# Optimization experiments

Hardware: AMD Instinct MI355X
Metric: run time of the kernel (lower is better)

The kernel has to match this reference:

```python
import jax, jax.numpy as jnp
import numpy as np

DIM = 384
NUM_HEADS = 6
HEAD_DIM = DIM // NUM_HEADS
SCALE = HEAD_DIM ** -0.5


def setup_inputs() -> dict:
    key = jax.random.key(0)
    k_x, k_wqkv, k_bqkv, k_wp, k_bp = jax.random.split(key, 5)
    B, N, D = 16, 1024, DIM
    s = 0.02
    return {
        "x": jax.random.normal(k_x, (B, N, D), dtype=jnp.float32),
        "w_qkv": jax.random.normal(k_wqkv, (D, 3 * D), dtype=jnp.float32) * s,
        "b_qkv": jax.random.normal(k_bqkv, (3 * D,), dtype=jnp.float32) * s,
        "w_proj": jax.random.normal(k_wp, (D, D), dtype=jnp.float32) * s,
        "b_proj": jax.random.normal(k_bp, (D,), dtype=jnp.float32) * s,
    }


def reference(x, w_qkv, b_qkv, w_proj, b_proj):
    b, n, d = x.shape
    qkv = x @ w_qkv + b_qkv                               # (B, N, 3D)
    qkv = qkv.reshape(b, n, 3, NUM_HEADS, HEAD_DIM)
    qkv = jnp.transpose(qkv, (2, 0, 3, 1, 4))             # (3, B, H, N, hd)
    q, k, v = qkv[0], qkv[1], qkv[2]
    attn = jnp.einsum("bhqd,bhkd->bhqk", q, k) * SCALE    # (B, H, N, N)
    attn = jax.nn.softmax(attn, axis=-1)
    out = jnp.einsum("bhqk,bhkd->bhqd", attn, v)          # (B, H, N, hd)
    out = jnp.transpose(out, (0, 2, 1, 3)).reshape(b, n, d)
    return out @ w_proj + b_proj
```

## Files before the change

### kernel.cpp

```cpp
#include <hip/hip_runtime.h>

typedef __attribute__((ext_vector_type(8))) short short8;
typedef __attribute__((ext_vector_type(4))) float float4_t;
typedef __attribute__((ext_vector_type(4))) unsigned int uint4_t;

#define MFMA16(A, B, C) __builtin_amdgcn_mfma_f32_16x16x32_bf16(A, B, C, 0, 0, 0)

#define QSCALE 0.1803368801111168f

__device__ __forceinline__ unsigned short f2bf(float f) {
  unsigned int u = __builtin_bit_cast(unsigned int, f);
  u += 0x7FFFu + ((u >> 16) & 1u);
  return (unsigned short)(u >> 16);
}

__device__ __forceinline__ void gload16(const unsigned short* g, unsigned short* l) {
  __builtin_amdgcn_global_load_lds(
      (const __attribute__((address_space(1))) unsigned int*)(g),
      (__attribute__((address_space(3))) unsigned int*)(l), 16, 0, 0);
}

__global__ __launch_bounds__(256) void prep(
    const float* __restrict__ w_qkv, const float* __restrict__ w_proj,
    unsigned short* __restrict__ wqkvT, unsigned short* __restrict__ wprojT) {
  __shared__ unsigned short tile[32][33];
  const int bid = blockIdx.x, tid = threadIdx.x;
  const float* w; unsigned short* wT; int E, t;
  if (bid < 432) { t = bid; w = w_qkv; wT = wqkvT; E = 1152; }
  else           { t = bid - 432; w = w_proj; wT = wprojT; E = 384; }
  const int tiles_e = E >> 5;
  const int td = t / tiles_e, te = t - td * tiles_e;
  const int r = tid >> 3, c4 = (tid & 7) * 4;
  float4 v = *reinterpret_cast<const float4*>(&w[(size_t)(td * 32 + r) * E + te * 32 + c4]);
  tile[r][c4 + 0] = f2bf(v.x);
  tile[r][c4 + 1] = f2bf(v.y);
  tile[r][c4 + 2] = f2bf(v.z);
  tile[r][c4 + 3] = f2bf(v.w);
  __syncthreads();
  ushort4 o;
  o.x = tile[c4 + 0][r]; o.y = tile[c4 + 1][r];
  o.z = tile[c4 + 2][r]; o.w = tile[c4 + 3][r];
  *reinterpret_cast<ushort4*>(&wT[(size_t)(te * 32 + r) * 384 + td * 32 + c4]) = o;
}

__global__ __launch_bounds__(256, 3) void gemm_qkv(
    const float* __restrict__ x,
    const unsigned short* __restrict__ wT,
    const float* __restrict__ bias,
    unsigned short* __restrict__ qb,
    unsigned short* __restrict__ kb,
    unsigned short* __restrict__ vt) {
  __shared__ alignas(16) char smem[49152];
  const int tid = threadIdx.x;
  const int wg = (blockIdx.x & 7) * 288 + (blockIdx.x >> 3);
  const int bm = wg / 18, bn = wg - bm * 18;
  const int m0 = bm * 128, n0 = bn * 64;
  const int lane = tid & 63, wid = tid >> 6;
  const int lr = lane & 15, lg = lane >> 4;
  const int wm = wid >> 1, wn = wid & 1;
  float4_t acc[4][2] = {};

  const float* xsrc[4];
  const unsigned short* bsrc[2];
  int adst[4], bdst[2];
#pragma unroll
  for (int i = 0; i < 4; ++i) {
    const int idx = tid + i * 256;
    const int r = idx >> 3, c8 = idx & 7;
    xsrc[i] = x + (size_t)(m0 + r) * 384 + (c8 ^ (r & 7)) * 8;
    adst[i] = idx * 16;
  }
#pragma unroll
  for (int i = 0; i < 2; ++i) {
    const int idx = tid + i * 256;
    const int r = idx >> 3, c8 = idx & 7;
    bsrc[i] = wT + (size_t)(n0 + r) * 384 + (c8 ^ (r & 7)) * 8;
    bdst[i] = idx * 16;
  }
  const int rxor = (lr & 7) << 4;

  float4 av[4][2];
  auto loadA = [&](int kt) {
#pragma unroll
    for (int i = 0; i < 4; ++i) {
      av[i][0] = *reinterpret_cast<const float4*>(xsrc[i] + kt * 64);
      av[i][1] = *reinterpret_cast<const float4*>(xsrc[i] + kt * 64 + 4);
    }
  };
  auto cvtWriteA = [&](char* abuf) {
#pragma unroll
    for (int i = 0; i < 4; ++i) {
      uint4_t u;
      u[0] = (unsigned int)f2bf(av[i][0].x) | ((unsigned int)f2bf(av[i][0].y) << 16);
      u[1] = (unsigned int)f2bf(av[i][0].z) | ((unsigned int)f2bf(av[i][0].w) << 16);
      u[2] = (unsigned int)f2bf(av[i][1].x) | ((unsigned int)f2bf(av[i][1].y) << 16);
      u[3] = (unsigned int)f2bf(av[i][1].z) | ((unsigned int)f2bf(av[i][1].w) << 16);
      *reinterpret_cast<uint4_t*>(abuf + adst[i]) = u;
    }
  };

  loadA(0);
#pragma unroll
  for (int i = 0; i < 2; ++i) gload16(bsrc[i], (unsigned short*)(smem + 32768 + bdst[i]));
  cvtWriteA(smem);
  __syncthreads();

#pragma unroll
  for (int kt = 0; kt < 6; ++kt) {
    const int cur = kt & 1;
    if (kt < 5) {
      loadA(kt + 1);
#pragma unroll
      for (int i = 0; i < 2; ++i)
        gload16(bsrc[i] + (kt + 1) * 64,
                (unsigned short*)(smem + 32768 + (cur ^ 1) * 8192 + bdst[i]));
    }
    const char* Ab = smem + cur * 16384;
    const char* Bb = smem + 32768 + cur * 8192;
#pragma unroll
    for (int kk = 0; kk < 2; ++kk) {
      short8 a[4], b[2];
#pragma unroll
      for (int f = 0; f < 4; ++f)
        a[f] = *reinterpret_cast<const short8*>(
            Ab + (wm * 64 + f * 16 + lr) * 128 + ((kk * 64 + lg * 16) ^ rxor));
#pragma unroll
      for (int f = 0; f < 2; ++f)
        b[f] = *reinterpret_cast<const short8*>(
            Bb + (wn * 32 + f * 16 + lr) * 128 + ((kk * 64 + lg * 16) ^ rxor));
      if (bn < 12) {
#pragma unroll
        for (int mf = 0; mf < 4; ++mf)
#pragma unroll
          for (int nf = 0; nf < 2; ++nf)
            acc[mf][nf] = MFMA16(b[nf], a[mf], acc[mf][nf]);
      } else {
#pragma unroll
        for (int mf = 0; mf < 4; ++mf)
#pragma unroll
          for (int nf = 0; nf < 2; ++nf)
            acc[mf][nf] = MFMA16(a[mf], b[nf], acc[mf][nf]);
      }
    }
    if (kt < 5) cvtWriteA(smem + (cur ^ 1) * 16384);
    __syncthreads();
  }

  if (bn < 12) {
    const int whichk = (bn >= 6);
    unsigned short* dst = whichk ? kb : qb;
    const float sc = whichk ? 1.f : QSCALE;
#pragma unroll
    for (int nf = 0; nf < 2; ++nf) {
      const int e0 = n0 + wn * 32 + nf * 16 + lg * 4;
      const int d0 = e0 - whichk * 384;
      const int h = d0 >> 6, hi0 = d0 & 63;
      const float4 bv4 = *reinterpret_cast<const float4*>(&bias[e0]);
#pragma unroll
      for (int mf = 0; mf < 4; ++mf) {
        const int mm = m0 + wm * 64 + mf * 16 + lr;
        const int b0 = mm >> 10, n_b = mm & 1023;
        const size_t bhh = (size_t)(b0 * 6 + h);
        ushort4 sv;
        sv.x = f2bf((acc[mf][nf][0] + bv4.x) * sc);
        sv.y = f2bf((acc[mf][nf][1] + bv4.y) * sc);
        sv.z = f2bf((acc[mf][nf][2] + bv4.z) * sc);
        sv.w = f2bf((acc[mf][nf][3] + bv4.w) * sc);
        *reinterpret_cast<ushort4*>(&dst[bhh * 65536 + (size_t)n_b * 64 + hi0]) = sv;
      }
    }
  } else {
#pragma unroll
    for (int nf = 0; nf < 2; ++nf) {
      const int e = n0 + wn * 32 + nf * 16 + lr;
      const float bv = bias[e];
      const int d = e - 768;
      const int h = d >> 6, hi = d & 63;
#pragma unroll
      for (int mf = 0; mf < 4; ++mf) {
        const int mm0 = m0 + wm * 64 + mf * 16 + lg * 4;
        const int b0 = mm0 >> 10, n_b = mm0 & 1023;
        const size_t bhh = (size_t)(b0 * 6 + h);
        const int np = (n_b & ~31) | ((n_b & 12) << 1) | ((n_b & 16) >> 2);
        ushort4 sv;
        sv.x = f2bf(acc[mf][nf][0] + bv);
        sv.y = f2bf(acc[mf][nf][1] + bv);
        sv.z = f2bf(acc[mf][nf][2] + bv);
        sv.w = f2bf(acc[mf][nf][3] + bv);
        *reinterpret_cast<ushort4*>(&vt[bhh * 65536 + (size_t)hi * 1024 + np]) = sv;
      }
    }
  }
}

__global__ __launch_bounds__(256, 3) void attn(
    const unsigned short* __restrict__ qb,
    const unsigned short* __restrict__ kb,
    const unsigned short* __restrict__ vt,
    unsigned short* __restrict__ ab) {
  __shared__ alignas(16) char smem[32768];
  const int tid = threadIdx.x;
  const int wg = (blockIdx.x & 7) * 96 + (blockIdx.x >> 3);
  const int bh = wg >> 3, qt = wg & 7;
  const int lane = tid & 63, wid = tid >> 6;
  const int lr = lane & 15, lg = lane >> 4;
  const size_t base = (size_t)bh * 65536;
  const unsigned short* qp = qb + base;
  const unsigned short* kp = kb + base;
  const unsigned short* vp = vt + base;
  const int q0 = qt * 128 + wid * 32;

  short8 aq[2][2];
#pragma unroll
  for (int qf = 0; qf < 2; ++qf)
#pragma unroll
    for (int h = 0; h < 2; ++h)
      aq[qf][h] = *reinterpret_cast<const short8*>(
          &qp[(size_t)(q0 + qf * 16 + lr) * 64 + h * 32 + lg * 8]);

  const unsigned short* ksrc[2];
  const unsigned short* vsrc[2];
  int soff[2];
#pragma unroll
  for (int i = 0; i < 2; ++i) {
    const int idx = tid + i * 256;
    const int r = idx >> 3, c8 = idx & 7;
    const int cc = (c8 ^ (r & 7)) * 8;
    ksrc[i] = kp + r * 64 + cc;
    vsrc[i] = vp + r * 1024 + cc;
    soff[i] = idx * 16;
  }
  const int xr = (lr & 7) << 4;

  float lsum0 = 0.f, lsum1 = 0.f;
  float4_t o0[4] = {}, o1[4] = {};

#pragma unroll
  for (int i = 0; i < 2; ++i) {
    gload16(ksrc[i], (unsigned short*)(smem + soff[i]));
    gload16(vsrc[i], (unsigned short*)(smem + 16384 + soff[i]));
  }
  __syncthreads();

  for (int kt = 0; kt < 16; ++kt) {
    const int cur = kt & 1;
    if (kt < 15) {
      const int nb = (cur ^ 1) * 8192;
#pragma unroll
      for (int i = 0; i < 2; ++i) {
        gload16(ksrc[i] + (kt + 1) * 4096, (unsigned short*)(smem + nb + soff[i]));
        gload16(vsrc[i] + (kt + 1) * 64, (unsigned short*)(smem + 16384 + nb + soff[i]));
      }
    }
    const char* kbase = smem + cur * 8192;
    const char* vbase = smem + 16384 + cur * 8192;

#pragma unroll
    for (int half = 0; half < 2; ++half) {
      short8 bk00 = *reinterpret_cast<const short8*>(
          kbase + (half * 32 + lr) * 128 + ((lg * 16) ^ xr));
      short8 bk01 = *reinterpret_cast<const short8*>(
          kbase + (half * 32 + lr) * 128 + ((64 + lg * 16) ^ xr));
      short8 bk10 = *reinterpret_cast<const short8*>(
          kbase + (half * 32 + 16 + lr) * 128 + ((lg * 16) ^ xr));
      short8 bk11 = *reinterpret_cast<const short8*>(
          kbase + (half * 32 + 16 + lr) * 128 + ((64 + lg * 16) ^ xr));
      short8 bv0 = *reinterpret_cast<const short8*>(
          vbase + (0 * 16 + lr) * 128 + ((half * 64 + lg * 16) ^ xr));
      short8 bv1 = *reinterpret_cast<const short8*>(
          vbase + (1 * 16 + lr) * 128 + ((half * 64 + lg * 16) ^ xr));
      short8 bv2 = *reinterpret_cast<const short8*>(
          vbase + (2 * 16 + lr) * 128 + ((half * 64 + lg * 16) ^ xr));
      short8 bv3 = *reinterpret_cast<const short8*>(
          vbase + (3 * 16 + lr) * 128 + ((half * 64 + lg * 16) ^ xr));

#pragma unroll
      for (int qf = 0; qf < 2; ++qf) {
        float4_t s0 = {}, s1 = {};
        __builtin_amdgcn_s_setprio(1);
        s0 = MFMA16(bk00, aq[qf][0], s0);
        s0 = MFMA16(bk01, aq[qf][1], s0);
        s1 = MFMA16(bk10, aq[qf][0], s1);
        s1 = MFMA16(bk11, aq[qf][1], s1);
        __builtin_amdgcn_s_setprio(0);

        unsigned int dw0, dw1, dw2, dw3;
        {
          const float p0 = __builtin_amdgcn_exp2f(s0[0]);
          const float p1 = __builtin_amdgcn_exp2f(s0[1]);
          const float p2 = __builtin_amdgcn_exp2f(s0[2]);
          const float p3 = __builtin_amdgcn_exp2f(s0[3]);
          asm("v_cvt_pk_bf16_f32 %0, %1, %2" : "=v"(dw0) : "v"(p0), "v"(p1));
          asm("v_cvt_pk_bf16_f32 %0, %1, %2" : "=v"(dw1) : "v"(p2), "v"(p3));
          const float p4 = __builtin_amdgcn_exp2f(s1[0]);
          const float p5 = __builtin_amdgcn_exp2f(s1[1]);
          const float p6 = __builtin_amdgcn_exp2f(s1[2]);
          const float p7 = __builtin_amdgcn_exp2f(s1[3]);
          asm("v_cvt_pk_bf16_f32 %0, %1, %2" : "=v"(dw2) : "v"(p4), "v"(p5));
          asm("v_cvt_pk_bf16_f32 %0, %1, %2" : "=v"(dw3) : "v"(p6), "v"(p7));
        }
        const float t0 = __builtin_bit_cast(float, dw0 << 16) +
                         __builtin_bit_cast(float, dw0 & 0xFFFF0000u);
        const float t1 = __builtin_bit_cast(float, dw1 << 16) +
                         __builtin_bit_cast(float, dw1 & 0xFFFF0000u);
        const float t2 = __builtin_bit_cast(float, dw2 << 16) +
                         __builtin_bit_cast(float, dw2 & 0xFFFF0000u);
        const float t3 = __builtin_bit_cast(float, dw3 << 16) +
                         __builtin_bit_cast(float, dw3 & 0xFFFF0000u);
        if (qf == 0) lsum0 += (t0 + t1) + (t2 + t3);
        else         lsum1 += (t0 + t1) + (t2 + t3);

        uint4_t pw;
        pw[0] = dw0; pw[1] = dw1; pw[2] = dw2; pw[3] = dw3;
        const short8 pa = __builtin_bit_cast(short8, pw);
        float4_t* o = (qf == 0) ? o0 : o1;
        __builtin_amdgcn_s_setprio(1);
        o[0] = MFMA16(pa, bv0, o[0]);
        o[1] = MFMA16(pa, bv1, o[1]);
        o[2] = MFMA16(pa, bv2, o[2]);
        o[3] = MFMA16(pa, bv3, o[3]);
        __builtin_amdgcn_s_setprio(0);
      }
    }
    __syncthreads();
  }

  float ti0 = lsum0, ti1 = lsum1;
  ti0 += __shfl_xor(ti0, 16);
  ti0 += __shfl_xor(ti0, 32);
  ti1 += __shfl_xor(ti1, 16);
  ti1 += __shfl_xor(ti1, 32);
  const float inv0 = 1.f / ti0;
  const float inv1 = 1.f / ti1;

  const int b = bh / 6, h = bh - b * 6;
#pragma unroll
  for (int qf = 0; qf < 2; ++qf) {
    const float4_t* o = (qf == 0) ? o0 : o1;
    const float inv = (qf == 0) ? inv0 : inv1;
    float invj[4];
#pragma unroll
    for (int j = 0; j < 4; ++j)
      invj[j] = __shfl(inv, lg * 4 + j);
#pragma unroll
    for (int f = 0; f < 4; ++f)
#pragma unroll
      for (int j = 0; j < 4; ++j) {
        const int q = q0 + qf * 16 + lg * 4 + j;
        ab[(size_t)(b * 1024 + q) * 384 + h * 64 + f * 16 + lr] =
            f2bf(o[f][j] * invj[j]);
      }
  }
}

__global__ __launch_bounds__(256, 3) void gemm_proj(
    const unsigned short* __restrict__ ab,
    const unsigned short* __restrict__ wT,
    const float* __restrict__ bias,
    float* __restrict__ out) {
  __shared__ alignas(16) char smem[49152];
  const int tid = threadIdx.x;
  const int wg = (blockIdx.x & 7) * 96 + (blockIdx.x >> 3);
  const int bm = wg / 3, bn = wg - bm * 3;
  const int m0 = bm * 64, n0 = bn * 128;
  const int lane = tid & 63, wid = tid >> 6;
  const int lr = lane & 15, lg = lane >> 4;
  const int wm = wid >> 1, wn = wid & 1;
  float4_t acc[2][4] = {};

  const unsigned short* asrc[2];
  const unsigned short* bsrc[4];
  int adst[2], bdst[4];
#pragma unroll
  for (int i = 0; i < 2; ++i) {
    const int idx = tid + i * 256;
    const int r = idx >> 3, c8 = idx & 7;
    asrc[i] = ab + (size_t)(m0 + r) * 384 + (c8 ^ (r & 7)) * 8;
    adst[i] = idx * 16;
  }
#pragma unroll
  for (int i = 0; i < 4; ++i) {
    const int idx = tid + i * 256;
    const int r = idx >> 3, c8 = idx & 7;
    bsrc[i] = wT + (size_t)(n0 + r) * 384 + (c8 ^ (r & 7)) * 8;
    bdst[i] = idx * 16;
  }
  const int rxor = (lr & 7) << 4;

#pragma unroll
  for (int i = 0; i < 2; ++i) gload16(asrc[i], (unsigned short*)(smem + adst[i]));
#pragma unroll
  for (int i = 0; i < 4; ++i) gload16(bsrc[i], (unsigned short*)(smem + 16384 + bdst[i]));
  __syncthreads();

#pragma unroll
  for (int kt = 0; kt < 6; ++kt) {
    const int cur = kt & 1;
    if (kt < 5) {
#pragma unroll
      for (int i = 0; i < 2; ++i)
        gload16(asrc[i] + (kt + 1) * 64, (unsigned short*)(smem + (cur ^ 1) * 8192 + adst[i]));
#pragma unroll
      for (int i = 0; i < 4; ++i)
        gload16(bsrc[i] + (kt + 1) * 64, (unsigned short*)(smem + 16384 + (cur ^ 1) * 16384 + bdst[i]));
    }
    const char* Ab = smem + cur * 8192;
    const char* Bb = smem + 16384 + cur * 16384;
#pragma unroll
    for (int kk = 0; kk < 2; ++kk) {
      short8 a[2], b[4];
#pragma unroll
      for (int f = 0; f < 2; ++f)
        a[f] = *reinterpret_cast<const short8*>(
            Ab + (wm * 32 + f * 16 + lr) * 128 + ((kk * 64 + lg * 16) ^ rxor));
#pragma unroll
      for (int f = 0; f < 4; ++f)
        b[f] = *reinterpret_cast<const short8*>(
            Bb + (wn * 64 + f * 16 + lr) * 128 + ((kk * 64 + lg * 16) ^ rxor));
#pragma unroll
      for (int mf = 0; mf < 2; ++mf)
#pragma unroll
        for (int nf = 0; nf < 4; ++nf)
          acc[mf][nf] = MFMA16(b[nf], a[mf], acc[mf][nf]);
    }
    __syncthreads();
  }

#pragma unroll
  for (int nf = 0; nf < 4; ++nf) {
    const int e0 = n0 + wn * 64 + nf * 16 + lg * 4;
    const float4 bv4 = *reinterpret_cast<const float4*>(&bias[e0]);
#pragma unroll
    for (int mf = 0; mf < 2; ++mf) {
      const int mm = m0 + wm * 32 + mf * 16 + lr;
      float4 ov;
      ov.x = acc[mf][nf][0] + bv4.x;
      ov.y = acc[mf][nf][1] + bv4.y;
      ov.z = acc[mf][nf][2] + bv4.z;
      ov.w = acc[mf][nf][3] + bv4.w;
      *reinterpret_cast<float4*>(&out[(size_t)mm * 384 + e0]) = ov;
    }
  }
}

extern "C" void kernel_launch(void* const* d_in, const int* in_sizes, int n_in,
                              void* d_out, int out_size, void* d_ws, size_t ws_size,
                              hipStream_t stream) {
  const float* x      = (const float*)d_in[0];
  const float* w_qkv  = (const float*)d_in[1];
  const float* b_qkv  = (const float*)d_in[2];
  const float* w_proj = (const float*)d_in[3];
  const float* b_proj = (const float*)d_in[4];
  float* out = (float*)d_out;

  char* ws = (char*)d_ws;
  unsigned short* ab     = (unsigned short*)(ws);
  unsigned short* wqkvT  = (unsigned short*)(ws + 12582912);
  unsigned short* wprojT = (unsigned short*)(ws + 13467648);
  unsigned short* qb     = (unsigned short*)(ws + 13762560);
  unsigned short* kb     = (unsigned short*)(ws + 26345472);
  unsigned short* vt     = (unsigned short*)(ws + 38928384);

  prep<<<576, 256, 0, stream>>>(w_qkv, w_proj, wqkvT, wprojT);
  gemm_qkv<<<2304, 256, 0, stream>>>(x, wqkvT, b_qkv, qb, kb, vt);
  attn<<<768, 256, 0, stream>>>(qb, kb, vt, ab);
  gemm_proj<<<768, 256, 0, stream>>>(ab, wprojT, b_proj, out);
}
```

Measured before the change: 92.98 us.

## Stream fp32 x directly into LDS and convert to bf16 at fragment load

The QKV GEMM now copies fp32 x tiles straight into LDS with async global_load_lds, instead of staging them through registers and converting to bf16 before the LDS write. Conversion moves to fragment read time using v_cvt_pk_bf16_f32, with a new swizzle for the 256-byte fp32 rows. This doubles the A buffer size (LDS grows to 80KB, occupancy hint drops from 3 to 2) and repeats the conversion for every warp that reads a row. Separately, the s_setprio hints around the MFMAs in the attention kernel are removed.

```diff
diff --git a/kernel.cpp b/kernel.cpp
--- a/kernel.cpp
+++ b/kernel.cpp
@@ -14,7 +14,7 @@
   return (unsigned short)(u >> 16);
 }
 
-__device__ __forceinline__ void gload16(const unsigned short* g, unsigned short* l) {
+__device__ __forceinline__ void gload16(const void* g, void* l) {
   __builtin_amdgcn_global_load_lds(
       (const __attribute__((address_space(1))) unsigned int*)(g),
       (__attribute__((address_space(3))) unsigned int*)(l), 16, 0, 0);
@@ -43,14 +43,14 @@
   *reinterpret_cast<ushort4*>(&wT[(size_t)(te * 32 + r) * 384 + td * 32 + c4]) = o;
 }
 
-__global__ __launch_bounds__(256, 3) void gemm_qkv(
+__global__ __launch_bounds__(256, 2) void gemm_qkv(
     const float* __restrict__ x,
     const unsigned short* __restrict__ wT,
     const float* __restrict__ bias,
     unsigned short* __restrict__ qb,
     unsigned short* __restrict__ kb,
     unsigned short* __restrict__ vt) {
-  __shared__ alignas(16) char smem[49152];
+  __shared__ alignas(16) char smem[81920];
   const int tid = threadIdx.x;
   const int wg = (blockIdx.x & 7) * 288 + (blockIdx.x >> 3);
   const int bm = wg / 18, bn = wg - bm * 18;
@@ -60,16 +60,17 @@
   const int wm = wid >> 1, wn = wid & 1;
   float4_t acc[4][2] = {};
 
-  const float* xsrc[4];
+  const float* asrc[8];
+  int adst[8];
+#pragma unroll
+  for (int i = 0; i < 8; ++i) {
+    const int idx = tid + i * 256;
+    const int r = idx >> 4, c = idx & 15;
+    asrc[i] = x + (size_t)(m0 + r) * 384 + ((c ^ ((r & 7) << 1)) << 2);
+    adst[i] = idx * 16;
+  }
   const unsigned short* bsrc[2];
-  int adst[4], bdst[2];
-#pragma unroll
-  for (int i = 0; i < 4; ++i) {
-    const int idx = tid + i * 256;
-    const int r = idx >> 3, c8 = idx & 7;
-    xsrc[i] = x + (size_t)(m0 + r) * 384 + (c8 ^ (r & 7)) * 8;
-    adst[i] = idx * 16;
-  }
+  int bdst[2];
 #pragma unroll
   for (int i = 0; i < 2; ++i) {
     const int idx = tid + i * 256;
@@ -77,57 +78,51 @@
     bsrc[i] = wT + (size_t)(n0 + r) * 384 + (c8 ^ (r & 7)) * 8;
     bdst[i] = idx * 16;
   }
-  const int rxor = (lr & 7) << 4;
-
-  float4 av[4][2];
-  auto loadA = [&](int kt) {
-#pragma unroll
-    for (int i = 0; i < 4; ++i) {
-      av[i][0] = *reinterpret_cast<const float4*>(xsrc[i] + kt * 64);
-      av[i][1] = *reinterpret_cast<const float4*>(xsrc[i] + kt * 64 + 4);
-    }
+  const int rxorB = (lr & 7) << 4;
+
+  auto loadA = [&](const char* Ab, int kk, int f) -> short8 {
+    const int row = wm * 64 + f * 16 + lr;
+    const int off = row * 256 + ((kk * 128 + lg * 32) ^ ((row & 7) << 5));
+    const float4_t x0 = *reinterpret_cast<const float4_t*>(Ab + off);
+    const float4_t x1 = *reinterpret_cast<const float4_t*>(Ab + off + 16);
+    unsigned int d0, d1, d2, d3;
+    asm("v_cvt_pk_bf16_f32 %0, %1, %2" : "=v"(d0) : "v"(x0[0]), "v"(x0[1]));
+    asm("v_cvt_pk_bf16_f32 %0, %1, %2" : "=v"(d1) : "v"(x0[2]), "v"(x0[3]));
+    asm("v_cvt_pk_bf16_f32 %0, %1, %2" : "=v"(d2) : "v"(x1[0]), "v"(x1[1]));
+    asm("v_cvt_pk_bf16_f32 %0, %1, %2" : "=v"(d3) : "v"(x1[2]), "v"(x1[3]));
+    uint4_t u;
+    u[0] = d0; u[1] = d1; u[2] = d2; u[3] = d3;
+    return __builtin_bit_cast(short8, u);
   };
-  auto cvtWriteA = [&](char* abuf) {
-#pragma unroll
-    for (int i = 0; i < 4; ++i) {
-      uint4_t u;
-      u[0] = (unsigned int)f2bf(av[i][0].x) | ((unsigned int)f2bf(av[i][0].y) << 16);
-      u[1] = (unsigned int)f2bf(av[i][0].z) | ((unsigned int)f2bf(av[i][0].w) << 16);
-      u[2] = (unsigned int)f2bf(av[i][1].x) | ((unsigned int)f2bf(av[i][1].y) << 16);
-      u[3] = (unsigned int)f2bf(av[i][1].z) | ((unsigned int)f2bf(av[i][1].w) << 16);
-      *reinterpret_cast<uint4_t*>(abuf + adst[i]) = u;
-    }
-  };
-
-  loadA(0);
-#pragma unroll
-  for (int i = 0; i < 2; ++i) gload16(bsrc[i], (unsigned short*)(smem + 32768 + bdst[i]));
-  cvtWriteA(smem);
+
+#pragma unroll
+  for (int i = 0; i < 8; ++i) gload16(asrc[i], smem + adst[i]);
+#pragma unroll
+  for (int i = 0; i < 2; ++i) gload16(bsrc[i], smem + 65536 + bdst[i]);
   __syncthreads();
 
 #pragma unroll
   for (int kt = 0; kt < 6; ++kt) {
     const int cur = kt & 1;
     if (kt < 5) {
-      loadA(kt + 1);
+#pragma unroll
+      for (int i = 0; i < 8; ++i)
+        gload16(asrc[i] + (kt + 1) * 64, smem + (cur ^ 1) * 32768 + adst[i]);
 #pragma unroll
       for (int i = 0; i < 2; ++i)
-        gload16(bsrc[i] + (kt + 1) * 64,
-                (unsigned short*)(smem + 32768 + (cur ^ 1) * 8192 + bdst[i]));
-    }
-    const char* Ab = smem + cur * 16384;
-    const char* Bb = smem + 32768 + cur * 8192;
+        gload16(bsrc[i] + (kt + 1) * 64, smem + 65536 + (cur ^ 1) * 8192 + bdst[i]);
+    }
+    const char* Ab = smem + cur * 32768;
+    const char* Bb = smem + 65536 + cur * 8192;
 #pragma unroll
     for (int kk = 0; kk < 2; ++kk) {
       short8 a[4], b[2];
 #pragma unroll
-      for (int f = 0; f < 4; ++f)
-        a[f] = *reinterpret_cast<const short8*>(
-            Ab + (wm * 64 + f * 16 + lr) * 128 + ((kk * 64 + lg * 16) ^ rxor));
+      for (int f = 0; f < 4; ++f) a[f] = loadA(Ab, kk, f);
 #pragma unroll
       for (int f = 0; f < 2; ++f)
         b[f] = *reinterpret_cast<const short8*>(
-            Bb + (wn * 32 + f * 16 + lr) * 128 + ((kk * 64 + lg * 16) ^ rxor));
+            Bb + (wn * 32 + f * 16 + lr) * 128 + ((kk * 64 + lg * 16) ^ rxorB));
       if (bn < 12) {
 #pragma unroll
         for (int mf = 0; mf < 4; ++mf)
@@ -142,7 +137,6 @@
             acc[mf][nf] = MFMA16(a[mf], b[nf], acc[mf][nf]);
       }
     }
-    if (kt < 5) cvtWriteA(smem + (cur ^ 1) * 16384);
     __syncthreads();
   }
 
@@ -237,8 +231,8 @@
 
 #pragma unroll
   for (int i = 0; i < 2; ++i) {
-    gload16(ksrc[i], (unsigned short*)(smem + soff[i]));
-    gload16(vsrc[i], (unsigned short*)(smem + 16384 + soff[i]));
+    gload16(ksrc[i], smem + soff[i]);
+    gload16(vsrc[i], smem + 16384 + soff[i]);
   }
   __syncthreads();
 
@@ -248,8 +242,8 @@
       const int nb = (cur ^ 1) * 8192;
 #pragma unroll
       for (int i = 0; i < 2; ++i) {
-        gload16(ksrc[i] + (kt + 1) * 4096, (unsigned short*)(smem + nb + soff[i]));
-        gload16(vsrc[i] + (kt + 1) * 64, (unsigned short*)(smem + 16384 + nb + soff[i]));
+        gload16(ksrc[i] + (kt + 1) * 4096, smem + nb + soff[i]);
+        gload16(vsrc[i] + (kt + 1) * 64, smem + 16384 + nb + soff[i]);
       }
     }
     const char* kbase = smem + cur * 8192;
@@ -277,12 +271,10 @@
 #pragma unroll
       for (int qf = 0; qf < 2; ++qf) {
         float4_t s0 = {}, s1 = {};
-        __builtin_amdgcn_s_setprio(1);
         s0 = MFMA16(bk00, aq[qf][0], s0);
         s0 = MFMA16(bk01, aq[qf][1], s0);
         s1 = MFMA16(bk10, aq[qf][0], s1);
         s1 = MFMA16(bk11, aq[qf][1], s1);
-        __builtin_amdgcn_s_setprio(0);
 
         unsigned int dw0, dw1, dw2, dw3;
         {
@@ -314,12 +306,10 @@
         pw[0] = dw0; pw[1] = dw1; pw[2] = dw2; pw[3] = dw3;
         const short8 pa = __builtin_bit_cast(short8, pw);
         float4_t* o = (qf == 0) ? o0 : o1;
-        __builtin_amdgcn_s_setprio(1);
         o[0] = MFMA16(pa, bv0, o[0]);
         o[1] = MFMA16(pa, bv1, o[1]);
         o[2] = MFMA16(pa, bv2, o[2]);
         o[3] = MFMA16(pa, bv3, o[3]);
-        __builtin_amdgcn_s_setprio(0);
       }
     }
     __syncthreads();
@@ -388,9 +378,9 @@
   const int rxor = (lr & 7) << 4;
 
 #pragma unroll
-  for (int i = 0; i < 2; ++i) gload16(asrc[i], (unsigned short*)(smem + adst[i]));
-#pragma unroll
-  for (int i = 0; i < 4; ++i) gload16(bsrc[i], (unsigned short*)(smem + 16384 + bdst[i]));
+  for (int i = 0; i < 2; ++i) gload16(asrc[i], smem + adst[i]);
+#pragma unroll
+  for (int i = 0; i < 4; ++i) gload16(bsrc[i], smem + 16384 + bdst[i]);
   __syncthreads();
 
 #pragma unroll
@@ -399,10 +389,10 @@
     if (kt < 5) {
 #pragma unroll
       for (int i = 0; i < 2; ++i)
-        gload16(asrc[i] + (kt + 1) * 64, (unsigned short*)(smem + (cur ^ 1) * 8192 + adst[i]));
+        gload16(asrc[i] + (kt + 1) * 64, smem + (cur ^ 1) * 8192 + adst[i]);
 #pragma unroll
       for (int i = 0; i < 4; ++i)
-        gload16(bsrc[i] + (kt + 1) * 64, (unsigned short*)(smem + 16384 + (cur ^ 1) * 16384 + bdst[i]));
+        gload16(bsrc[i] + (kt + 1) * 64, smem + 16384 + (cur ^ 1) * 16384 + bdst[i]);
     }
     const char* Ab = smem + cur * 8192;
     const char* Bb = smem + 16384 + cur * 16384;
```

Measured after the change: 95.68 us. +2.9%, slower.
